# Kernel tuning notes

Hardware: AMD Instinct MI355X
Metric: run time of the kernel (lower is better)

The kernel has to match this reference:

```python
import jax, jax.numpy as jnp
import numpy as np

N_MAX_BIG = 200  # number of basis terms
L_MAX = 50
PERIOD = 10.0


def setup_inputs() -> dict:
    key = jax.random.key(0)
    kx, ke = jax.random.split(key)
    x = jax.random.normal(kx, (1_000_000,), dtype=jnp.float32)
    eigenvectors = jax.random.normal(ke, (L_MAX + 1, N_MAX_BIG, N_MAX_BIG), dtype=jnp.float32)
    return {"n": 5, "l": 1, "x": x, "eigenvectors": eigenvectors}


def reference(n, l, x, eigenvectors):
    # coeff[m] = eigenvectors[l][m, n], shape [M]
    coeff = eigenvectors[l][:, n]
    m = jnp.arange(N_MAX_BIG, dtype=x.dtype)
    if l == 0:
        # c(m, x) = cos(pi * (m + 0.5) * x / 10)
        freqs = (jnp.pi / PERIOD) * (m + 0.5)           # [M]
        basis = jnp.cos(freqs[:, None] * x[None, :])    # [M, N]
    else:
        # s(m, x) = sin(pi * (m + 1) * x / 10)
        freqs = (jnp.pi / PERIOD) * (m + 1.0)           # [M]
        basis = jnp.sin(freqs[:, None] * x[None, :])    # [M, N]
    # ret = sum_m coeff[m] * basis[m, :]
    return jnp.einsum('m,mn->n', coeff, basis)
```

## Files before the change

### kernel.cpp

```cpp
#include <hip/hip_runtime.h>
#include <math.h>

#define MTERMS 200
#define EPT 8


__device__ __forceinline__ float cos_poly(float t2) {
    float c = 4.7794773e-14f;
    c = fmaf(c, t2, -1.1470746e-11f);
    c = fmaf(c, t2,  2.0876757e-9f);
    c = fmaf(c, t2, -2.7557319e-7f);
    c = fmaf(c, t2,  2.4801587e-5f);
    c = fmaf(c, t2, -1.3888889e-3f);
    c = fmaf(c, t2,  4.1666668e-2f);
    c = fmaf(c, t2, -0.5f);
    c = fmaf(c, t2,  1.0f);
    return c;
}

__device__ __forceinline__ float sin_poly(float t, float t2) {
    float s = -7.6471637e-13f;
    s = fmaf(s, t2,  1.6059044e-10f);
    s = fmaf(s, t2, -2.5052108e-8f);
    s = fmaf(s, t2,  2.7557319e-6f);
    s = fmaf(s, t2, -1.9841270e-4f);
    s = fmaf(s, t2,  8.3333333e-3f);
    s = fmaf(s, t2, -0.16666667f);
    s = fmaf(s, t2,  1.0f);
    return t * s;
}

__global__ __launch_bounds__(256, 2)
void physical_basis_kernel(const int* __restrict__ n_p,
                           const int* __restrict__ l_p,
                           const float* __restrict__ x,
                           const float* __restrict__ eig,
                           float* __restrict__ out,
                           int n_elem)
{
    __shared__ float4 scoef4[MTERMS / 4];
    float* scoef = reinterpret_cast<float*>(scoef4);

    const int n = n_p[0];
    const int l = l_p[0];

    for (int m = threadIdx.x; m < MTERMS; m += blockDim.x) {
        scoef[m] = eig[(size_t)l * (MTERMS * MTERMS) + (size_t)m * MTERMS + n];
    }
    __syncthreads();

    const int base = (blockIdx.x * blockDim.x + threadIdx.x) * EPT;
    if (base >= n_elem) return;

    const float kfreq = 0.31415926535897932384626f;

    float xe[EPT];
    const bool full = (base + EPT - 1) < n_elem;
    if (full) {
        float4 xa = *reinterpret_cast<const float4*>(x + base);
        float4 xb = *reinterpret_cast<const float4*>(x + base + 4);
        xe[0] = xa.x; xe[1] = xa.y; xe[2] = xa.z; xe[3] = xa.w;
        xe[4] = xb.x; xe[5] = xb.y; xe[6] = xb.z; xe[7] = xb.w;
    } else {
        #pragma unroll
        for (int j = 0; j < EPT; ++j)
            xe[j] = (base + j < n_elem) ? x[base + j] : 0.0f;
    }

    float fm[EPT], fm1[EPT], twoc[EPT], acc[EPT];

    #pragma unroll
    for (int e = 0; e < EPT; ++e) {
        float t  = kfreq * xe[e];
        float t2 = t * t;
        float c  = cos_poly(t2);
        twoc[e]  = 2.0f * c;
        if (l == 0) {
            float h = cos_poly(0.25f * t2);
            fm[e]  = h;
            fm1[e] = fmaf(twoc[e], h, -h);
        } else {
            float s = sin_poly(t, t2);
            fm[e]  = s;
            fm1[e] = twoc[e] * s;
        }
        acc[e] = 0.0f;
    }

    float4 cf = scoef4[0];
    #pragma unroll 1
    for (int mq = 0; mq < MTERMS / 4 - 1; ++mq) {
        float4 nxt = scoef4[mq + 1];
        float cfa[4] = {cf.x, cf.y, cf.z, cf.w};
        #pragma unroll
        for (int k = 0; k < 4; ++k) {
            #pragma unroll
            for (int e = 0; e < EPT; ++e) {
                acc[e] = fmaf(cfa[k], fm[e], acc[e]);
                float fn = fmaf(twoc[e], fm1[e], -fm[e]);
                fm[e]  = fm1[e];
                fm1[e] = fn;
            }
        }
        cf = nxt;
    }
    {
        float cfa[4] = {cf.x, cf.y, cf.z, cf.w};
        #pragma unroll
        for (int k = 0; k < 4; ++k) {
            #pragma unroll
            for (int e = 0; e < EPT; ++e) {
                acc[e] = fmaf(cfa[k], fm[e], acc[e]);
                float fn = fmaf(twoc[e], fm1[e], -fm[e]);
                fm[e]  = fm1[e];
                fm1[e] = fn;
            }
        }
    }

    if (full) {
        float4 oa, ob;
        oa.x = acc[0]; oa.y = acc[1]; oa.z = acc[2]; oa.w = acc[3];
        ob.x = acc[4]; ob.y = acc[5]; ob.z = acc[6]; ob.w = acc[7];
        *reinterpret_cast<float4*>(out + base)     = oa;
        *reinterpret_cast<float4*>(out + base + 4) = ob;
    } else {
        #pragma unroll
        for (int j = 0; j < EPT; ++j)
            if (base + j < n_elem) out[base + j] = acc[j];
    }
}

extern "C" void kernel_launch(void* const* d_in, const int* in_sizes, int n_in,
                              void* d_out, int out_size, void* d_ws, size_t ws_size,
                              hipStream_t stream) {
    const int*   n_p = (const int*)d_in[0];
    const int*   l_p = (const int*)d_in[1];
    const float* x   = (const float*)d_in[2];
    const float* eig = (const float*)d_in[3];
    float*       o   = (float*)d_out;

    const int n_elem  = in_sizes[2];
    const int threads = 256;
    const int blocks  = (n_elem + threads * EPT - 1) / (threads * EPT);

    hipLaunchKernelGGL(physical_basis_kernel, dim3(blocks), dim3(threads), 0, stream,
                       n_p, l_p, x, eig, o, n_elem);
}
```

Measured before the change: 75.26 us.

## Halve elements per thread, raise occupancy, and hoist x load before coefficient sync

Elements per thread drop from 8 to 4 and the launch bound rises to 4 blocks per CU, so twice as many threads run with fewer registers each. The load of x now starts before the shared-memory coefficient fill and the barrier, so its latency overlaps that setup. The Chebyshev recurrence uses two ping-pong registers in place of a shift-and-copy. The aim is more latency hiding and less stall, at the cost of less instruction-level parallelism per thread and twice as many blocks that each redo the coefficient fill.

```diff
diff --git a/kernel.cpp b/kernel.cpp
--- a/kernel.cpp
+++ b/kernel.cpp
@@ -2,7 +2,7 @@
 #include <math.h>
 
 #define MTERMS 200
-#define EPT 8
+#define EPT 4
 
 
 __device__ __forceinline__ float cos_poly(float t2) {
@@ -30,7 +30,31 @@
     return t * s;
 }
 
-__global__ __launch_bounds__(256, 2)
+#define QUAD_STEP(CF)                                                          \
+    do {                                                                       \
+        _Pragma("unroll")                                                      \
+        for (int e = 0; e < EPT; ++e) {                                        \
+            acc[e] = fmaf((CF).x, fa[e], acc[e]);                              \
+            fa[e]  = fmaf(twoc[e], fb[e], -fa[e]);                             \
+        }                                                                      \
+        _Pragma("unroll")                                                      \
+        for (int e = 0; e < EPT; ++e) {                                        \
+            acc[e] = fmaf((CF).y, fb[e], acc[e]);                              \
+            fb[e]  = fmaf(twoc[e], fa[e], -fb[e]);                             \
+        }                                                                      \
+        _Pragma("unroll")                                                      \
+        for (int e = 0; e < EPT; ++e) {                                        \
+            acc[e] = fmaf((CF).z, fa[e], acc[e]);                              \
+            fa[e]  = fmaf(twoc[e], fb[e], -fa[e]);                             \
+        }                                                                      \
+        _Pragma("unroll")                                                      \
+        for (int e = 0; e < EPT; ++e) {                                        \
+            acc[e] = fmaf((CF).w, fb[e], acc[e]);                              \
+            fb[e]  = fmaf(twoc[e], fa[e], -fb[e]);                             \
+        }                                                                      \
+    } while (0)
+
+__global__ __launch_bounds__(256, 4)
 void physical_basis_kernel(const int* __restrict__ n_p,
                            const int* __restrict__ l_p,
                            const float* __restrict__ x,
@@ -41,6 +65,22 @@
     __shared__ float4 scoef4[MTERMS / 4];
     float* scoef = reinterpret_cast<float*>(scoef4);
 
+    const int base = (blockIdx.x * blockDim.x + threadIdx.x) * EPT;
+    const bool active = base < n_elem;
+    const bool full   = (base + EPT - 1) < n_elem;
+
+    float xe[EPT];
+    #pragma unroll
+    for (int j = 0; j < EPT; ++j) xe[j] = 0.0f;
+    if (full) {
+        float4 xa = *reinterpret_cast<const float4*>(x + base);
+        xe[0] = xa.x; xe[1] = xa.y; xe[2] = xa.z; xe[3] = xa.w;
+    } else if (active) {
+        #pragma unroll
+        for (int j = 0; j < EPT; ++j)
+            if (base + j < n_elem) xe[j] = x[base + j];
+    }
+
     const int n = n_p[0];
     const int l = l_p[0];
 
@@ -49,25 +89,11 @@
     }
     __syncthreads();
 
-    const int base = (blockIdx.x * blockDim.x + threadIdx.x) * EPT;
-    if (base >= n_elem) return;
+    if (!active) return;
 
     const float kfreq = 0.31415926535897932384626f;
 
-    float xe[EPT];
-    const bool full = (base + EPT - 1) < n_elem;
-    if (full) {
-        float4 xa = *reinterpret_cast<const float4*>(x + base);
-        float4 xb = *reinterpret_cast<const float4*>(x + base + 4);
-        xe[0] = xa.x; xe[1] = xa.y; xe[2] = xa.z; xe[3] = xa.w;
-        xe[4] = xb.x; xe[5] = xb.y; xe[6] = xb.z; xe[7] = xb.w;
-    } else {
-        #pragma unroll
-        for (int j = 0; j < EPT; ++j)
-            xe[j] = (base + j < n_elem) ? x[base + j] : 0.0f;
-    }
-
-    float fm[EPT], fm1[EPT], twoc[EPT], acc[EPT];
+    float fa[EPT], fb[EPT], twoc[EPT], acc[EPT];
 
     #pragma unroll
     for (int e = 0; e < EPT; ++e) {
@@ -77,12 +103,12 @@
         twoc[e]  = 2.0f * c;
         if (l == 0) {
             float h = cos_poly(0.25f * t2);
-            fm[e]  = h;
-            fm1[e] = fmaf(twoc[e], h, -h);
+            fa[e] = h;
+            fb[e] = fmaf(twoc[e], h, -h);
         } else {
             float s = sin_poly(t, t2);
-            fm[e]  = s;
-            fm1[e] = twoc[e] * s;
+            fa[e] = s;
+            fb[e] = twoc[e] * s;
         }
         acc[e] = 0.0f;
     }
@@ -91,39 +117,15 @@
     #pragma unroll 1
     for (int mq = 0; mq < MTERMS / 4 - 1; ++mq) {
         float4 nxt = scoef4[mq + 1];
-        float cfa[4] = {cf.x, cf.y, cf.z, cf.w};
-        #pragma unroll
-        for (int k = 0; k < 4; ++k) {
-            #pragma unroll
-            for (int e = 0; e < EPT; ++e) {
-                acc[e] = fmaf(cfa[k], fm[e], acc[e]);
-                float fn = fmaf(twoc[e], fm1[e], -fm[e]);
-                fm[e]  = fm1[e];
-                fm1[e] = fn;
-            }
-        }
+        QUAD_STEP(cf);
         cf = nxt;
     }
-    {
-        float cfa[4] = {cf.x, cf.y, cf.z, cf.w};
-        #pragma unroll
-        for (int k = 0; k < 4; ++k) {
-            #pragma unroll
-            for (int e = 0; e < EPT; ++e) {
-                acc[e] = fmaf(cfa[k], fm[e], acc[e]);
-                float fn = fmaf(twoc[e], fm1[e], -fm[e]);
-                fm[e]  = fm1[e];
-                fm1[e] = fn;
-            }
-        }
-    }
+    QUAD_STEP(cf);
 
     if (full) {
-        float4 oa, ob;
+        float4 oa;
         oa.x = acc[0]; oa.y = acc[1]; oa.z = acc[2]; oa.w = acc[3];
-        ob.x = acc[4]; ob.y = acc[5]; ob.z = acc[6]; ob.w = acc[7];
-        *reinterpret_cast<float4*>(out + base)     = oa;
-        *reinterpret_cast<float4*>(out + base + 4) = ob;
+        *reinterpret_cast<float4*>(out + base) = oa;
     } else {
         #pragma unroll
         for (int j = 0; j < EPT; ++j)
```

New measurement: 76.39 us. About the same (+1.5%).
